# Optimization experiments

Hardware: AMD Instinct MI355X
Metric: run time of the kernel (lower is better)

The kernel has to match this reference:

```python
import jax, jax.numpy as jnp
import numpy as np


def setup_inputs() -> dict:
    key = jax.random.key(0)
    ks = jax.random.split(key, 8)
    B, C, H, W = 4, 256, 64, 64
    Cqk = C // 8
    s = 1.0 / np.sqrt(C)
    return {
        "x": jax.random.normal(ks[0], (B, C, H, W), jnp.float32),
        "wq": jax.random.normal(ks[1], (Cqk, C), jnp.float32) * s,
        "bq": jax.random.normal(ks[2], (Cqk,), jnp.float32) * 0.01,
        "wk": jax.random.normal(ks[3], (Cqk, C), jnp.float32) * s,
        "bk": jax.random.normal(ks[4], (Cqk,), jnp.float32) * 0.01,
        "wv": jax.random.normal(ks[5], (C, C), jnp.float32) * s,
        "bv": jax.random.normal(ks[6], (C,), jnp.float32) * 0.01,
        "gamma": jax.random.normal(ks[7], (1,), jnp.float32),
    }


def reference(x, wq, bq, wk, bk, wv, bv, gamma):
    B, C, H, W = x.shape
    N = H * W
    xf = x.reshape(B, C, N)  # [B, C, N]
    # 1x1 convs are per-pixel channel matmuls
    q = jnp.einsum('oc,bcn->bon', wq, xf) + bq[None, :, None]  # [B, C//8, N]
    k = jnp.einsum('oc,bcn->bon', wk, xf) + bk[None, :, None]  # [B, C//8, N]
    v = jnp.einsum('oc,bcn->bon', wv, xf) + bv[None, :, None]  # [B, C, N]
    # energy[b, n, m] = q[b,:,n] . k[b,:,m]  (unscaled)
    energy = jnp.einsum('bcn,bcm->bnm', q, k)  # [B, N, N]
    # original applies softmax over dim=-2, i.e. over the query index n per column m
    attn = jax.nn.softmax(energy, axis=-2)  # [B, N, N]
    at_map = jnp.transpose(attn, (0, 2, 1))  # returned map, [B, N, N]
    # sa_map = V @ attn : bmm([B,C,N],[B,N,N]) -> [B,C,N]
    sa = jnp.einsum('bcn,bnm->bcm', v, attn).reshape(B, C, H, W)
    out = x + gamma[0] * sa
    return (out, at_map)
```

## Files before the change

### kernel.cpp

```cpp
#include <hip/hip_runtime.h>
#include <hip/hip_bf16.h>
#include <cstdint>
#include <cstddef>

#define NPIX 4096
#define CIN  256
#define CQK  32
#define BSZ  4

typedef __attribute__((ext_vector_type(8))) short          bf16x8;
typedef __attribute__((ext_vector_type(4))) float          f32x4;
typedef __attribute__((ext_vector_type(8))) unsigned short u16x8;

static __device__ inline unsigned short f2bf(float f) {
    __hip_bfloat16 h = __float2bfloat16(f);
    unsigned short u;
    __builtin_memcpy(&u, &h, 2);
    return u;
}

static __device__ inline void gl2lds16(const void* g, void* l) {
    __builtin_amdgcn_global_load_lds(
        (const __attribute__((address_space(1))) unsigned int*)g,
        (__attribute__((address_space(3))) unsigned int*)l,
        16, 0, 0);
}

__global__ __launch_bounds__(256) void proj_kernel(
    const float* __restrict__ x, const float* __restrict__ W,
    const float* __restrict__ bias, float* __restrict__ y, int Cout)
{
    __shared__ float Wl[8][CIN];
    const int t  = threadIdx.x;
    const int n0 = blockIdx.x * 1024;
    const int o0 = blockIdx.y * 8;
    const int b  = blockIdx.z;

    #pragma unroll
    for (int j = 0; j < 8; ++j) {
        int flat = t + 256 * j;
        int row = flat >> 8, col = flat & 255;
        Wl[row][col] = W[(o0 + row) * CIN + col];
    }
    __syncthreads();

    float acc[8][4];
    #pragma unroll
    for (int o = 0; o < 8; ++o)
        #pragma unroll
        for (int i = 0; i < 4; ++i) acc[o][i] = 0.f;

    const float* xb = x + ((size_t)b * CIN) * NPIX + n0 + t * 4;
    #pragma unroll 4
    for (int c = 0; c < CIN; ++c) {
        float4 xv = *(const float4*)(xb + (size_t)c * NPIX);
        #pragma unroll
        for (int o = 0; o < 8; ++o) {
            float w = Wl[o][c];
            acc[o][0] = fmaf(w, xv.x, acc[o][0]);
            acc[o][1] = fmaf(w, xv.y, acc[o][1]);
            acc[o][2] = fmaf(w, xv.z, acc[o][2]);
            acc[o][3] = fmaf(w, xv.w, acc[o][3]);
        }
    }
    #pragma unroll
    for (int o = 0; o < 8; ++o) {
        float bb = bias[o0 + o];
        float4 r = { acc[o][0] + bb, acc[o][1] + bb,
                     acc[o][2] + bb, acc[o][3] + bb };
        *(float4*)(y + ((size_t)(b * Cout + o0 + o)) * NPIX + n0 + t * 4) = r;
    }
}

__global__ __launch_bounds__(256) void proj_bf16_kernel(
    const float* __restrict__ x, const float* __restrict__ W,
    const float* __restrict__ bias, unsigned short* __restrict__ y, int Cout)
{
    __shared__ float Wl[8][CIN];
    const int t  = threadIdx.x;
    const int n0 = blockIdx.x * 1024;
    const int o0 = blockIdx.y * 8;
    const int b  = blockIdx.z;

    #pragma unroll
    for (int j = 0; j < 8; ++j) {
        int flat = t + 256 * j;
        int row = flat >> 8, col = flat & 255;
        Wl[row][col] = W[(o0 + row) * CIN + col];
    }
    __syncthreads();

    float acc[8][4];
    #pragma unroll
    for (int o = 0; o < 8; ++o)
        #pragma unroll
        for (int i = 0; i < 4; ++i) acc[o][i] = 0.f;

    const float* xb = x + ((size_t)b * CIN) * NPIX + n0 + t * 4;
    #pragma unroll 4
    for (int c = 0; c < CIN; ++c) {
        float4 xv = *(const float4*)(xb + (size_t)c * NPIX);
        #pragma unroll
        for (int o = 0; o < 8; ++o) {
            float w = Wl[o][c];
            acc[o][0] = fmaf(w, xv.x, acc[o][0]);
            acc[o][1] = fmaf(w, xv.y, acc[o][1]);
            acc[o][2] = fmaf(w, xv.z, acc[o][2]);
            acc[o][3] = fmaf(w, xv.w, acc[o][3]);
        }
    }
    #pragma unroll
    for (int o = 0; o < 8; ++o) {
        float bb = bias[o0 + o];
        ushort4 r;
        r.x = f2bf(acc[o][0] + bb);
        r.y = f2bf(acc[o][1] + bb);
        r.z = f2bf(acc[o][2] + bb);
        r.w = f2bf(acc[o][3] + bb);
        *(ushort4*)(y + ((size_t)(b * Cout + o0 + o)) * NPIX + n0 + t * 4) = r;
    }
}

__global__ __launch_bounds__(512) void energy_softmax_kernel(
    const float* __restrict__ q, const float* __restrict__ k,
    float* __restrict__ at_map, unsigned short* __restrict__ attn_bf)
{
    __shared__ float kk[8][CQK];
    __shared__ float wred[8];
    const int t  = threadIdx.x;
    const int m0 = blockIdx.x * 8;
    const int b  = blockIdx.y;
    const int lane = t & 63, wid = t >> 6;

    if (t < 256) {
        int c = t >> 3, mi = t & 7;
        kk[mi][c] = k[((size_t)(b * CQK + c)) * NPIX + m0 + mi];
    }
    __syncthreads();

    float s[8][8];
    #pragma unroll
    for (int mi = 0; mi < 8; ++mi)
        #pragma unroll
        for (int i = 0; i < 8; ++i) s[mi][i] = 0.f;

    const float* qb = q + ((size_t)b * CQK) * NPIX + t * 8;
    #pragma unroll 2
    for (int c = 0; c < CQK; ++c) {
        float4 q0 = *(const float4*)(qb + (size_t)c * NPIX);
        float4 q1 = *(const float4*)(qb + (size_t)c * NPIX + 4);
        #pragma unroll
        for (int mi = 0; mi < 8; ++mi) {
            float w = kk[mi][c];
            s[mi][0] = fmaf(w, q0.x, s[mi][0]);
            s[mi][1] = fmaf(w, q0.y, s[mi][1]);
            s[mi][2] = fmaf(w, q0.z, s[mi][2]);
            s[mi][3] = fmaf(w, q0.w, s[mi][3]);
            s[mi][4] = fmaf(w, q1.x, s[mi][4]);
            s[mi][5] = fmaf(w, q1.y, s[mi][5]);
            s[mi][6] = fmaf(w, q1.z, s[mi][6]);
            s[mi][7] = fmaf(w, q1.w, s[mi][7]);
        }
    }

    #pragma unroll
    for (int mi = 0; mi < 8; ++mi) {
        float mx = s[mi][0];
        #pragma unroll
        for (int i = 1; i < 8; ++i) mx = fmaxf(mx, s[mi][i]);
        #pragma unroll
        for (int off = 1; off < 64; off <<= 1)
            mx = fmaxf(mx, __shfl_xor(mx, off, 64));
        if (lane == 0) wred[wid] = mx;
        __syncthreads();
        float bmx = wred[0];
        #pragma unroll
        for (int w = 1; w < 8; ++w) bmx = fmaxf(bmx, wred[w]);
        __syncthreads();

        float sum = 0.f;
        #pragma unroll
        for (int i = 0; i < 8; ++i) {
            s[mi][i] = __expf(s[mi][i] - bmx);
            sum += s[mi][i];
        }
        #pragma unroll
        for (int off = 1; off < 64; off <<= 1)
            sum += __shfl_xor(sum, off, 64);
        if (lane == 0) wred[wid] = sum;
        __syncthreads();
        float bsum = 0.f;
        #pragma unroll
        for (int w = 0; w < 8; ++w) bsum += wred[w];
        __syncthreads();

        float inv = 1.f / bsum;
        size_t rowoff = ((size_t)(b * NPIX) + m0 + mi) * NPIX + t * 8;
        float a0 = s[mi][0]*inv, a1 = s[mi][1]*inv, a2 = s[mi][2]*inv, a3 = s[mi][3]*inv;
        float a4 = s[mi][4]*inv, a5 = s[mi][5]*inv, a6 = s[mi][6]*inv, a7 = s[mi][7]*inv;
        float4 r0 = { a0, a1, a2, a3 };
        float4 r1 = { a4, a5, a6, a7 };
        *(float4*)(at_map + rowoff)     = r0;
        *(float4*)(at_map + rowoff + 4) = r1;
        if (attn_bf) {
            u16x8 rb;
            rb[0] = f2bf(a0); rb[1] = f2bf(a1); rb[2] = f2bf(a2); rb[3] = f2bf(a3);
            rb[4] = f2bf(a4); rb[5] = f2bf(a5); rb[6] = f2bf(a6); rb[7] = f2bf(a7);
            *(u16x8*)(attn_bf + rowoff) = rb;
        }
    }
}

__global__ __launch_bounds__(256) void sa_gemm_mfma(
    const unsigned short* __restrict__ v,
    const unsigned short* __restrict__ attn,
    const float* __restrict__ x, const float* __restrict__ gptr,
    float* __restrict__ out)
{
    __shared__ __align__(16) unsigned short As[128 * 64];
    __shared__ __align__(16) unsigned short Bs[128 * 64];

    const int t = threadIdx.x, lane = t & 63, w = t >> 6;
    const int m_base = blockIdx.x * 128;
    const int c_base = blockIdx.y * 128;
    const int b      = blockIdx.z;
    const int wc = (w >> 1) * 64, wm = (w & 1) * 64;

    const int lrow = lane >> 3;
    const int glog = (lane & 7) ^ lrow;
    const unsigned short* aSrc[4];
    const unsigned short* bSrc[4];
    #pragma unroll
    for (int qi = 0; qi < 4; ++qi) {
        int r = w * 32 + qi * 8 + lrow;
        aSrc[qi] = v    + ((size_t)(b * CIN + c_base + r)) * NPIX + glog * 8;
        bSrc[qi] = attn + ((size_t)b * NPIX + m_base + r) * NPIX + glog * 8;
    }

    const int l15 = lane & 15, q4 = lane >> 4;
    const int x0 = (q4 ^ (lane & 7)) * 8;
    const int x1 = ((q4 ^ 4) ^ (lane & 7)) * 8;
    const int baseA = (wc + l15) * 64;
    const int baseB = (wm + l15) * 64;

    f32x4 acc[4][4];
    #pragma unroll
    for (int i = 0; i < 4; ++i)
        #pragma unroll
        for (int j = 0; j < 4; ++j) acc[i][j] = (f32x4)(0.0f);

    for (int k0 = 0; k0 < NPIX; k0 += 64) {
        #pragma unroll
        for (int qi = 0; qi < 4; ++qi) {
            gl2lds16(aSrc[qi] + k0, &As[(w * 32 + qi * 8) * 64]);
            gl2lds16(bSrc[qi] + k0, &Bs[(w * 32 + qi * 8) * 64]);
        }
        __syncthreads();
        #pragma unroll
        for (int ks = 0; ks < 2; ++ks) {
            const int xo = ks ? x1 : x0;
            bf16x8 af[4], bfr[4];
            #pragma unroll
            for (int i = 0; i < 4; ++i)
                af[i] = *(const bf16x8*)&As[baseA + i * 1024 + xo];
            #pragma unroll
            for (int j = 0; j < 4; ++j)
                bfr[j] = *(const bf16x8*)&Bs[baseB + j * 1024 + xo];
            #pragma unroll
            for (int i = 0; i < 4; ++i)
                #pragma unroll
                for (int j = 0; j < 4; ++j)
                    acc[i][j] = __builtin_amdgcn_mfma_f32_16x16x32_bf16(
                        af[i], bfr[j], acc[i][j], 0, 0, 0);
        }
        __syncthreads();
    }

    const float g = gptr[0];
    #pragma unroll
    for (int i = 0; i < 4; ++i) {
        int c = c_base + wc + i * 16 + q4 * 4;
        #pragma unroll
        for (int j = 0; j < 4; ++j) {
            int m = m_base + wm + j * 16 + l15;
            #pragma unroll
            for (int r = 0; r < 4; ++r) {
                size_t idx = ((size_t)(b * CIN + c + r)) * NPIX + m;
                out[idx] = x[idx] + g * acc[i][j][r];
            }
        }
    }
}

__global__ __launch_bounds__(256) void sa_gemm_kernel(
    const float* __restrict__ v, const float* __restrict__ at_map,
    const float* __restrict__ x, const float* __restrict__ gptr,
    float* __restrict__ out)
{
    __shared__ float Vt[32][68];
    __shared__ float At[32][68];
    const int t  = threadIdx.x;
    const int m0 = blockIdx.x * 64;
    const int c0 = blockIdx.y * 64;
    const int b  = blockIdx.z;
    const int r  = t >> 2, qd = t & 3;
    const int tc = t & 15, tm = t >> 4;

    const float* vb = v      + ((size_t)(b * CIN  + c0 + r)) * NPIX + qd * 4;
    const float* ab = at_map + ((size_t)(b * NPIX + m0 + r)) * NPIX + qd * 4;

    float acc[4][4];
    #pragma unroll
    for (int i = 0; i < 4; ++i)
        #pragma unroll
        for (int j = 0; j < 4; ++j) acc[i][j] = 0.f;

    for (int n0 = 0; n0 < NPIX; n0 += 32) {
        float4 v0 = *(const float4*)(vb + n0);
        float4 v1 = *(const float4*)(vb + n0 + 16);
        float4 a0 = *(const float4*)(ab + n0);
        float4 a1 = *(const float4*)(ab + n0 + 16);
        Vt[qd*4+0][r] = v0.x; Vt[qd*4+1][r] = v0.y;
        Vt[qd*4+2][r] = v0.z; Vt[qd*4+3][r] = v0.w;
        Vt[16+qd*4+0][r] = v1.x; Vt[16+qd*4+1][r] = v1.y;
        Vt[16+qd*4+2][r] = v1.z; Vt[16+qd*4+3][r] = v1.w;
        At[qd*4+0][r] = a0.x; At[qd*4+1][r] = a0.y;
        At[qd*4+2][r] = a0.z; At[qd*4+3][r] = a0.w;
        At[16+qd*4+0][r] = a1.x; At[16+qd*4+1][r] = a1.y;
        At[16+qd*4+2][r] = a1.z; At[16+qd*4+3][r] = a1.w;
        __syncthreads();
        #pragma unroll
        for (int kk = 0; kk < 32; ++kk) {
            float4 a  = *(const float4*)&Vt[kk][tc * 4];
            float4 bb = *(const float4*)&At[kk][tm * 4];
            acc[0][0] = fmaf(a.x, bb.x, acc[0][0]);
            acc[0][1] = fmaf(a.x, bb.y, acc[0][1]);
            acc[0][2] = fmaf(a.x, bb.z, acc[0][2]);
            acc[0][3] = fmaf(a.x, bb.w, acc[0][3]);
            acc[1][0] = fmaf(a.y, bb.x, acc[1][0]);
            acc[1][1] = fmaf(a.y, bb.y, acc[1][1]);
            acc[1][2] = fmaf(a.y, bb.z, acc[1][2]);
            acc[1][3] = fmaf(a.y, bb.w, acc[1][3]);
            acc[2][0] = fmaf(a.z, bb.x, acc[2][0]);
            acc[2][1] = fmaf(a.z, bb.y, acc[2][1]);
            acc[2][2] = fmaf(a.z, bb.z, acc[2][2]);
            acc[2][3] = fmaf(a.z, bb.w, acc[2][3]);
            acc[3][0] = fmaf(a.w, bb.x, acc[3][0]);
            acc[3][1] = fmaf(a.w, bb.y, acc[3][1]);
            acc[3][2] = fmaf(a.w, bb.z, acc[3][2]);
            acc[3][3] = fmaf(a.w, bb.w, acc[3][3]);
        }
        __syncthreads();
    }

    const float g = *gptr;
    #pragma unroll
    for (int i = 0; i < 4; ++i) {
        size_t row = ((size_t)(b * CIN + c0 + tc * 4 + i)) * NPIX + m0 + tm * 4;
        float4 xv = *(const float4*)(x + row);
        float4 o  = { xv.x + g * acc[i][0], xv.y + g * acc[i][1],
                      xv.z + g * acc[i][2], xv.w + g * acc[i][3] };
        *(float4*)(out + row) = o;
    }
}

extern "C" void kernel_launch(void* const* d_in, const int* in_sizes, int n_in,
                              void* d_out, int out_size, void* d_ws, size_t ws_size,
                              hipStream_t stream) {
    const float* x     = (const float*)d_in[0];
    const float* wq    = (const float*)d_in[1];
    const float* bq    = (const float*)d_in[2];
    const float* wk    = (const float*)d_in[3];
    const float* bk    = (const float*)d_in[4];
    const float* wv    = (const float*)d_in[5];
    const float* bv    = (const float*)d_in[6];
    const float* gamma = (const float*)d_in[7];

    float* out    = (float*)d_out;
    float* at_map = out + (size_t)BSZ * CIN * NPIX;

    const size_t qk_elems  = (size_t)BSZ * CQK * NPIX;
    const size_t v_elems   = (size_t)BSZ * CIN * NPIX;
    const size_t nn_elems  = (size_t)BSZ * NPIX * NPIX;

    const size_t need_fast = 2 * qk_elems * 4 + v_elems * 2 + nn_elems * 2;

    if (ws_size >= need_fast) {
        float*          q       = (float*)d_ws;
        float*          k       = q + qk_elems;
        unsigned short* v_bf    = (unsigned short*)(k + qk_elems);
        unsigned short* attn_bf = v_bf + v_elems;

        proj_kernel<<<dim3(NPIX/1024, CQK/8, BSZ), 256, 0, stream>>>(x, wq, bq, q, CQK);
        proj_kernel<<<dim3(NPIX/1024, CQK/8, BSZ), 256, 0, stream>>>(x, wk, bk, k, CQK);
        proj_bf16_kernel<<<dim3(NPIX/1024, CIN/8, BSZ), 256, 0, stream>>>(x, wv, bv, v_bf, CIN);

        energy_softmax_kernel<<<dim3(NPIX/8, BSZ), 512, 0, stream>>>(q, k, at_map, attn_bf);

        sa_gemm_mfma<<<dim3(NPIX/128, CIN/128, BSZ), 256, 0, stream>>>(
            v_bf, attn_bf, x, gamma, out);
    } else {
        float* q = (float*)d_ws;
        float* k = q + qk_elems;
        float* v = k + qk_elems;

        proj_kernel<<<dim3(NPIX/1024, CQK/8, BSZ), 256, 0, stream>>>(x, wq, bq, q, CQK);
        proj_kernel<<<dim3(NPIX/1024, CQK/8, BSZ), 256, 0, stream>>>(x, wk, bk, k, CQK);
        proj_kernel<<<dim3(NPIX/1024, CIN/8, BSZ), 256, 0, stream>>>(x, wv, bv, v, CIN);

        energy_softmax_kernel<<<dim3(NPIX/8, BSZ), 512, 0, stream>>>(q, k, at_map, nullptr);

        sa_gemm_kernel<<<dim3(NPIX/64, CIN/64, BSZ), 256, 0, stream>>>(
            v, at_map, x, gamma, out);
    }
}
```

Measured before the change: 625.7 us.

## Merge Q/K projections, batch softmax reductions, shrink GEMM tile, add nontemporal stores

```diff
diff --git a/kernel.cpp b/kernel.cpp
--- a/kernel.cpp
+++ b/kernel.cpp
@@ -72,52 +72,104 @@
     }
 }
 
-__global__ __launch_bounds__(256) void proj_bf16_kernel(
-    const float* __restrict__ x, const float* __restrict__ W,
-    const float* __restrict__ bias, unsigned short* __restrict__ y, int Cout)
-{
-    __shared__ float Wl[8][CIN];
+__global__ __launch_bounds__(256) void proj_qk_kernel(
+    const float* __restrict__ x,
+    const float* __restrict__ wq, const float* __restrict__ bq,
+    const float* __restrict__ wk, const float* __restrict__ bk,
+    float* __restrict__ qout, float* __restrict__ kout)
+{
+    __shared__ float Wl[CIN][12];
     const int t  = threadIdx.x;
-    const int n0 = blockIdx.x * 1024;
-    const int o0 = blockIdx.y * 8;
+    const int n0 = blockIdx.x * 512;
+    const int og = blockIdx.y * 8;
     const int b  = blockIdx.z;
+    const bool isK = og >= CQK;
+    const float* W    = isK ? wk : wq;
+    const float* bias = isK ? bk : bq;
+    float* y          = isK ? kout : qout;
+    const int o0      = isK ? og - CQK : og;
 
     #pragma unroll
     for (int j = 0; j < 8; ++j) {
         int flat = t + 256 * j;
-        int row = flat >> 8, col = flat & 255;
-        Wl[row][col] = W[(o0 + row) * CIN + col];
-    }
-    __syncthreads();
-
-    float acc[8][4];
-    #pragma unroll
-    for (int o = 0; o < 8; ++o)
-        #pragma unroll
-        for (int i = 0; i < 4; ++i) acc[o][i] = 0.f;
-
-    const float* xb = x + ((size_t)b * CIN) * NPIX + n0 + t * 4;
+        int o = flat >> 8, c = flat & 255;
+        Wl[c][o] = W[(o0 + o) * CIN + c];
+    }
+    __syncthreads();
+
+    float acc[8][2];
+    #pragma unroll
+    for (int o = 0; o < 8; ++o) { acc[o][0] = 0.f; acc[o][1] = 0.f; }
+
+    const float* xb = x + ((size_t)b * CIN) * NPIX + n0 + t * 2;
     #pragma unroll 4
     for (int c = 0; c < CIN; ++c) {
-        float4 xv = *(const float4*)(xb + (size_t)c * NPIX);
+        float2 xv = *(const float2*)(xb + (size_t)c * NPIX);
+        f32x4 w0 = *(const f32x4*)&Wl[c][0];
+        f32x4 w1 = *(const f32x4*)&Wl[c][4];
+        float wv[8] = { w0[0], w0[1], w0[2], w0[3],
+                        w1[0], w1[1], w1[2], w1[3] };
         #pragma unroll
         for (int o = 0; o < 8; ++o) {
-            float w = Wl[o][c];
-            acc[o][0] = fmaf(w, xv.x, acc[o][0]);
-            acc[o][1] = fmaf(w, xv.y, acc[o][1]);
-            acc[o][2] = fmaf(w, xv.z, acc[o][2]);
-            acc[o][3] = fmaf(w, xv.w, acc[o][3]);
+            acc[o][0] = fmaf(wv[o], xv.x, acc[o][0]);
+            acc[o][1] = fmaf(wv[o], xv.y, acc[o][1]);
         }
     }
     #pragma unroll
     for (int o = 0; o < 8; ++o) {
         float bb = bias[o0 + o];
-        ushort4 r;
+        float2 r = { acc[o][0] + bb, acc[o][1] + bb };
+        *(float2*)(y + ((size_t)(b * CQK + o0 + o)) * NPIX + n0 + t * 2) = r;
+    }
+}
+
+__global__ __launch_bounds__(256) void proj_v_bf16_kernel(
+    const float* __restrict__ x, const float* __restrict__ W,
+    const float* __restrict__ bias, unsigned short* __restrict__ y)
+{
+    __shared__ float Wl[CIN][20];
+    const int t  = threadIdx.x;
+    const int n0 = blockIdx.x * 512;
+    const int o0 = blockIdx.y * 16;
+    const int b  = blockIdx.z;
+
+    #pragma unroll
+    for (int j = 0; j < 16; ++j) {
+        int flat = t + 256 * j;
+        int o = flat >> 8, c = flat & 255;
+        Wl[c][o] = W[(o0 + o) * CIN + c];
+    }
+    __syncthreads();
+
+    float acc[16][2];
+    #pragma unroll
+    for (int o = 0; o < 16; ++o) { acc[o][0] = 0.f; acc[o][1] = 0.f; }
+
+    const float* xb = x + ((size_t)b * CIN) * NPIX + n0 + t * 2;
+    #pragma unroll 2
+    for (int c = 0; c < CIN; ++c) {
+        float2 xv = *(const float2*)(xb + (size_t)c * NPIX);
+        f32x4 w0 = *(const f32x4*)&Wl[c][0];
+        f32x4 w1 = *(const f32x4*)&Wl[c][4];
+        f32x4 w2 = *(const f32x4*)&Wl[c][8];
+        f32x4 w3 = *(const f32x4*)&Wl[c][12];
+        float wv[16] = { w0[0], w0[1], w0[2], w0[3],
+                         w1[0], w1[1], w1[2], w1[3],
+                         w2[0], w2[1], w2[2], w2[3],
+                         w3[0], w3[1], w3[2], w3[3] };
+        #pragma unroll
+        for (int o = 0; o < 16; ++o) {
+            acc[o][0] = fmaf(wv[o], xv.x, acc[o][0]);
+            acc[o][1] = fmaf(wv[o], xv.y, acc[o][1]);
+        }
+    }
+    #pragma unroll
+    for (int o = 0; o < 16; ++o) {
+        float bb = bias[o0 + o];
+        ushort2 r;
         r.x = f2bf(acc[o][0] + bb);
         r.y = f2bf(acc[o][1] + bb);
-        r.z = f2bf(acc[o][2] + bb);
-        r.w = f2bf(acc[o][3] + bb);
-        *(ushort4*)(y + ((size_t)(b * Cout + o0 + o)) * NPIX + n0 + t * 4) = r;
+        *(ushort2*)(y + ((size_t)(b * CIN + o0 + o)) * NPIX + n0 + t * 2) = r;
     }
 }
 
@@ -125,8 +177,9 @@
     const float* __restrict__ q, const float* __restrict__ k,
     float* __restrict__ at_map, unsigned short* __restrict__ attn_bf)
 {
-    __shared__ float kk[8][CQK];
-    __shared__ float wred[8];
+    __shared__ float kk[CQK][12];
+    __shared__ float wredM[8][8];
+    __shared__ float wredS[8][8];
     const int t  = threadIdx.x;
     const int m0 = blockIdx.x * 8;
     const int b  = blockIdx.y;
@@ -134,7 +187,7 @@
 
     if (t < 256) {
         int c = t >> 3, mi = t & 7;
-        kk[mi][c] = k[((size_t)(b * CQK + c)) * NPIX + m0 + mi];
+        kk[c][mi] = k[((size_t)(b * CQK + c)) * NPIX + m0 + mi];
     }
     __syncthreads();
 
@@ -149,9 +202,13 @@
     for (int c = 0; c < CQK; ++c) {
         float4 q0 = *(const float4*)(qb + (size_t)c * NPIX);
         float4 q1 = *(const float4*)(qb + (size_t)c * NPIX + 4);
+        f32x4 k0 = *(const f32x4*)&kk[c][0];
+        f32x4 k1 = *(const f32x4*)&kk[c][4];
+        float kv[8] = { k0[0], k0[1], k0[2], k0[3],
+                        k1[0], k1[1], k1[2], k1[3] };
         #pragma unroll
         for (int mi = 0; mi < 8; ++mi) {
-            float w = kk[mi][c];
+            float w = kv[mi];
             s[mi][0] = fmaf(w, q0.x, s[mi][0]);
             s[mi][1] = fmaf(w, q0.y, s[mi][1]);
             s[mi][2] = fmaf(w, q0.z, s[mi][2]);
@@ -171,13 +228,15 @@
         #pragma unroll
         for (int off = 1; off < 64; off <<= 1)
             mx = fmaxf(mx, __shfl_xor(mx, off, 64));
-        if (lane == 0) wred[wid] = mx;
-        __syncthreads();
-        float bmx = wred[0];
-        #pragma unroll
-        for (int w = 1; w < 8; ++w) bmx = fmaxf(bmx, wred[w]);
-        __syncthreads();
-
+        if (lane == 0) wredM[mi][wid] = mx;
+    }
+    __syncthreads();
+
+    #pragma unroll
+    for (int mi = 0; mi < 8; ++mi) {
+        float bmx = wredM[mi][0];
+        #pragma unroll
+        for (int w = 1; w < 8; ++w) bmx = fmaxf(bmx, wredM[mi][w]);
         float sum = 0.f;
         #pragma unroll
         for (int i = 0; i < 8; ++i) {
@@ -187,21 +246,23 @@
         #pragma unroll
         for (int off = 1; off < 64; off <<= 1)
             sum += __shfl_xor(sum, off, 64);
-        if (lane == 0) wred[wid] = sum;
-        __syncthreads();
+        if (lane == 0) wredS[mi][wid] = sum;
+    }
+    __syncthreads();
+
+    #pragma unroll
+    for (int mi = 0; mi < 8; ++mi) {
         float bsum = 0.f;
         #pragma unroll
-        for (int w = 0; w < 8; ++w) bsum += wred[w];
-        __syncthreads();
-
+        for (int w = 0; w < 8; ++w) bsum += wredS[mi][w];
         float inv = 1.f / bsum;
         size_t rowoff = ((size_t)(b * NPIX) + m0 + mi) * NPIX + t * 8;
         float a0 = s[mi][0]*inv, a1 = s[mi][1]*inv, a2 = s[mi][2]*inv, a3 = s[mi][3]*inv;
         float a4 = s[mi][4]*inv, a5 = s[mi][5]*inv, a6 = s[mi][6]*inv, a7 = s[mi][7]*inv;
-        float4 r0 = { a0, a1, a2, a3 };
-        float4 r1 = { a4, a5, a6, a7 };
-        *(float4*)(at_map + rowoff)     = r0;
-        *(float4*)(at_map + rowoff + 4) = r1;
+        f32x4 r0 = { a0, a1, a2, a3 };
+        f32x4 r1 = { a4, a5, a6, a7 };
+        __builtin_nontemporal_store(r0, (f32x4*)(at_map + rowoff));
+        __builtin_nontemporal_store(r1, (f32x4*)(at_map + rowoff + 4));
         if (attn_bf) {
             u16x8 rb;
             rb[0] = f2bf(a0); rb[1] = f2bf(a1); rb[2] = f2bf(a2); rb[3] = f2bf(a3);
@@ -218,24 +279,24 @@
     float* __restrict__ out)
 {
     __shared__ __align__(16) unsigned short As[128 * 64];
-    __shared__ __align__(16) unsigned short Bs[128 * 64];
+    __shared__ __align__(16) unsigned short Bs[64 * 64];
 
     const int t = threadIdx.x, lane = t & 63, w = t >> 6;
-    const int m_base = blockIdx.x * 128;
+    const int m_base = blockIdx.x * 64;
     const int c_base = blockIdx.y * 128;
     const int b      = blockIdx.z;
-    const int wc = (w >> 1) * 64, wm = (w & 1) * 64;
+    const int wc = (w >> 1) * 64, wm = (w & 1) * 32;
 
     const int lrow = lane >> 3;
     const int glog = (lane & 7) ^ lrow;
     const unsigned short* aSrc[4];
-    const unsigned short* bSrc[4];
-    #pragma unroll
-    for (int qi = 0; qi < 4; ++qi) {
-        int r = w * 32 + qi * 8 + lrow;
-        aSrc[qi] = v    + ((size_t)(b * CIN + c_base + r)) * NPIX + glog * 8;
-        bSrc[qi] = attn + ((size_t)b * NPIX + m_base + r) * NPIX + glog * 8;
-    }
+    const unsigned short* bSrc[2];
+    #pragma unroll
+    for (int qi = 0; qi < 4; ++qi)
+        aSrc[qi] = v    + ((size_t)(b * CIN + c_base + w * 32 + qi * 8 + lrow)) * NPIX + glog * 8;
+    #pragma unroll
+    for (int qi = 0; qi < 2; ++qi)
+        bSrc[qi] = attn + ((size_t)b * NPIX + m_base + w * 16 + qi * 8 + lrow) * NPIX + glog * 8;
 
     const int l15 = lane & 15, q4 = lane >> 4;
     const int x0 = (q4 ^ (lane & 7)) * 8;
@@ -243,33 +304,34 @@
     const int baseA = (wc + l15) * 64;
     const int baseB = (wm + l15) * 64;
 
-    f32x4 acc[4][4];
+    f32x4 acc[4][2];
     #pragma unroll
     for (int i = 0; i < 4; ++i)
         #pragma unroll
-        for (int j = 0; j < 4; ++j) acc[i][j] = (f32x4)(0.0f);
+        for (int j = 0; j < 2; ++j) acc[i][j] = (f32x4)(0.0f);
 
     for (int k0 = 0; k0 < NPIX; k0 += 64) {
         #pragma unroll
-        for (int qi = 0; qi < 4; ++qi) {
+        for (int qi = 0; qi < 4; ++qi)
             gl2lds16(aSrc[qi] + k0, &As[(w * 32 + qi * 8) * 64]);
-            gl2lds16(bSrc[qi] + k0, &Bs[(w * 32 + qi * 8) * 64]);
-        }
+        #pragma unroll
+        for (int qi = 0; qi < 2; ++qi)
+            gl2lds16(bSrc[qi] + k0, &Bs[(w * 16 + qi * 8) * 64]);
         __syncthreads();
         #pragma unroll
         for (int ks = 0; ks < 2; ++ks) {
             const int xo = ks ? x1 : x0;
-            bf16x8 af[4], bfr[4];
+            bf16x8 af[4], bfr[2];
             #pragma unroll
             for (int i = 0; i < 4; ++i)
                 af[i] = *(const bf16x8*)&As[baseA + i * 1024 + xo];
             #pragma unroll
-            for (int j = 0; j < 4; ++j)
+            for (int j = 0; j < 2; ++j)
                 bfr[j] = *(const bf16x8*)&Bs[baseB + j * 1024 + xo];
             #pragma unroll
             for (int i = 0; i < 4; ++i)
                 #pragma unroll
-                for (int j = 0; j < 4; ++j)
+                for (int j = 0; j < 2; ++j)
                     acc[i][j] = __builtin_amdgcn_mfma_f32_16x16x32_bf16(
                         af[i], bfr[j], acc[i][j], 0, 0, 0);
         }
@@ -281,12 +343,13 @@
     for (int i = 0; i < 4; ++i) {
         int c = c_base + wc + i * 16 + q4 * 4;
         #pragma unroll
-        for (int j = 0; j < 4; ++j) {
+        for (int j = 0; j < 2; ++j) {
             int m = m_base + wm + j * 16 + l15;
             #pragma unroll
             for (int r = 0; r < 4; ++r) {
                 size_t idx = ((size_t)(b * CIN + c + r)) * NPIX + m;
-                out[idx] = x[idx] + g * acc[i][j][r];
+                float val = x[idx] + g * acc[i][j][r];
+                __builtin_nontemporal_store(val, &out[idx]);
             }
         }
     }
@@ -391,13 +454,14 @@
         unsigned short* v_bf    = (unsigned short*)(k + qk_elems);
         unsigned short* attn_bf = v_bf + v_elems;
 
-        proj_kernel<<<dim3(NPIX/1024, CQK/8, BSZ), 256, 0, stream>>>(x, wq, bq, q, CQK);
-        proj_kernel<<<dim3(NPIX/1024, CQK/8, BSZ), 256, 0, stream>>>(x, wk, bk, k, CQK);
-        proj_bf16_kernel<<<dim3(NPIX/1024, CIN/8, BSZ), 256, 0, stream>>>(x, wv, bv, v_bf, CIN);
+        proj_qk_kernel<<<dim3(NPIX/512, 8, BSZ), 256, 0, stream>>>(
+            x, wq, bq, wk, bk, q, k);
+        proj_v_bf16_kernel<<<dim3(NPIX/512, CIN/16, BSZ), 256, 0, stream>>>(
+            x, wv, bv, v_bf);
 
         energy_softmax_kernel<<<dim3(NPIX/8, BSZ), 512, 0, stream>>>(q, k, at_map, attn_bf);
 
-        sa_gemm_mfma<<<dim3(NPIX/128, CIN/128, BSZ), 256, 0, stream>>>(
+        sa_gemm_mfma<<<dim3(NPIX/64, CIN/128, BSZ), 256, 0, stream>>>(
             v_bf, attn_bf, x, gamma, out);
     } else {
         float* q = (float*)d_ws;
```

Measured after the change: 566.2 us. 9.5% less time.
